# Kernel optimization log

Hardware: AMD Instinct MI355X
Metric: run time of the kernel (lower is better)

## Reference

```python
import jax, jax.numpy as jnp
import numpy as np

EMBED_DIM = 1024
HIDDEN_DIM = 4096
NUM_EXPERTS = 8
TOP_K = 2


def setup_inputs() -> dict:
    key = jax.random.key(0)
    ks = jax.random.split(key, 5)
    x = jax.random.normal(ks[0], (2, 2048, EMBED_DIM), dtype=jnp.float32)
    Wg = jax.random.normal(ks[1], (EMBED_DIM, NUM_EXPERTS), dtype=jnp.float32) * 0.02
    W1 = jax.random.normal(ks[2], (NUM_EXPERTS, EMBED_DIM, HIDDEN_DIM), dtype=jnp.float32) * 0.02
    W3 = jax.random.normal(ks[3], (NUM_EXPERTS, EMBED_DIM, HIDDEN_DIM), dtype=jnp.float32) * 0.02
    W2 = jax.random.normal(ks[4], (NUM_EXPERTS, HIDDEN_DIM, EMBED_DIM), dtype=jnp.float32) * 0.02
    return {"x": x, "Wg": Wg, "W1": W1, "W3": W3, "W2": W2}


def reference(x, Wg, W1, W3, W2):
    # Gate: linear projection to num_experts logits
    gate = jnp.einsum("bsd,de->bse", x, Wg)  # [B,S,E]
    top_vals, top_idx = jax.lax.top_k(gate, TOP_K)  # [B,S,K]
    sel_w = jax.nn.softmax(top_vals, axis=-1)  # softmax over top-k values
    # Scatter selected weights into dense [B,S,E] (zeros for unselected experts)
    dense_w = jnp.sum(
        jax.nn.one_hot(top_idx, NUM_EXPERTS, dtype=sel_w.dtype) * sel_w[..., None],
        axis=-2,
    )  # [B,S,E]
    # Per-expert SwiGLU FFN; weight=0 for tokens not routed to expert e,
    # so the weighted-sum form is mathematically identical to masked dispatch.
    out = jnp.zeros_like(x)
    for e in range(NUM_EXPERTS):
        h = jax.nn.swish(jnp.einsum("bsd,dh->bsh", x, W1[e])) * jnp.einsum(
            "bsd,dh->bsh", x, W3[e]
        )
        out = out + dense_w[..., e:e + 1] * jnp.einsum("bsh,hd->bsd", h, W2[e])
    return out
```

## Files before the change

kernel.cpp:

```cpp
#include <hip/hip_runtime.h>
#include <hip/hip_bf16.h>
#include <stdint.h>

#define D_EMBED 1024
#define D_HID   4096
#define N_TOK   4096
#define N_EXP   8
#define CAP     4096
#define NROWA   8320

typedef __attribute__((ext_vector_type(4))) float f32x4;
typedef __attribute__((ext_vector_type(8))) short bf16x8;

__device__ __forceinline__ unsigned short f2bf(float f) {
    unsigned int u = __builtin_bit_cast(unsigned int, f);
    u += 0x7fffu + ((u >> 16) & 1u);
    return (unsigned short)(u >> 16);
}

__device__ __forceinline__ void gload_lds16(const void* g, void* l) {
    __builtin_amdgcn_global_load_lds(
        (const __attribute__((address_space(1))) unsigned int*)g,
        (__attribute__((address_space(3))) unsigned int*)l,
        16, 0, 0);
}

__global__ __launch_bounds__(256) void pack_w(const float* __restrict__ W,
                                              unsigned short* __restrict__ out, int R, int C) {
    int e = blockIdx.z, kb = blockIdx.y, cb = blockIdx.x;
    const float* Wp = W + (size_t)e * R * C + (size_t)(kb * 64) * C + cb * 64;
    unsigned short* op = out + (size_t)e * R * C;
    __shared__ unsigned short lds[64][72];
    int t = threadIdx.x;
    int r = t >> 2;
    int c0 = (t & 3) << 4;
    const float* src = Wp + (size_t)r * C + c0;
#pragma unroll
    for (int i = 0; i < 2; ++i) {
        f32x4 a = *reinterpret_cast<const f32x4*>(src + i * 8);
        f32x4 b = *reinterpret_cast<const f32x4*>(src + i * 8 + 4);
        bf16x8 o;
        o[0]=(short)f2bf(a[0]); o[1]=(short)f2bf(a[1]); o[2]=(short)f2bf(a[2]); o[3]=(short)f2bf(a[3]);
        o[4]=(short)f2bf(b[0]); o[5]=(short)f2bf(b[1]); o[6]=(short)f2bf(b[2]); o[7]=(short)f2bf(b[3]);
        *reinterpret_cast<bf16x8*>(&lds[r][c0 + i * 8]) = o;
    }
    __syncthreads();
#pragma unroll
    for (int i = 0; i < 2; ++i) {
        int cell = i * 256 + t;
        int ksl = cell >> 6, col = cell & 63;
        bf16x8 o;
#pragma unroll
        for (int j = 0; j < 8; ++j) o[j] = (short)lds[ksl * 8 + j][col];
        *reinterpret_cast<bf16x8*>(op + ((size_t)(kb * 8 + ksl) * C + cb * 64 + col) * 8) = o;
    }
}

__global__ __launch_bounds__(256) void gate_kernel(const float* __restrict__ x,
                                                   const float* __restrict__ Wg,
                                                   int* __restrict__ counts,
                                                   int* __restrict__ toks,
                                                   float* __restrict__ wgts,
                                                   int* __restrict__ slots) {
    int wave = threadIdx.x >> 6;
    int lane = threadIdx.x & 63;
    int tok = blockIdx.x * 4 + wave;
    const float* xp = x + (size_t)tok * D_EMBED;
    float acc[8] = {0, 0, 0, 0, 0, 0, 0, 0};
#pragma unroll
    for (int i = 0; i < 16; ++i) {
        int d = lane + 64 * i;
        float xv = xp[d];
        f32x4 w0 = *reinterpret_cast<const f32x4*>(Wg + (size_t)d * 8);
        f32x4 w1 = *reinterpret_cast<const f32x4*>(Wg + (size_t)d * 8 + 4);
        acc[0] += xv * w0[0]; acc[1] += xv * w0[1]; acc[2] += xv * w0[2]; acc[3] += xv * w0[3];
        acc[4] += xv * w1[0]; acc[5] += xv * w1[1]; acc[6] += xv * w1[2]; acc[7] += xv * w1[3];
    }
#pragma unroll
    for (int e = 0; e < 8; ++e)
        for (int s = 32; s; s >>= 1) acc[e] += __shfl_xor(acc[e], s, 64);
    if (lane == 0) {
        int i0 = 0; float v0 = acc[0];
#pragma unroll
        for (int e = 1; e < 8; ++e) if (acc[e] > v0) { v0 = acc[e]; i0 = e; }
        int i1 = -1; float v1 = -1e30f;
#pragma unroll
        for (int e = 0; e < 8; ++e) if (e != i0 && acc[e] > v1) { v1 = acc[e]; i1 = e; }
        float ex = __expf(v1 - v0);
        float w0 = 1.0f / (1.0f + ex);
        float w1 = 1.0f - w0;
        int p0 = atomicAdd(&counts[i0], 1);
        toks[i0 * CAP + p0] = tok; wgts[i0 * CAP + p0] = w0; slots[i0 * CAP + p0] = 0;
        int p1 = atomicAdd(&counts[i1], 1);
        toks[i1 * CAP + p1] = tok; wgts[i1 * CAP + p1] = w1; slots[i1 * CAP + p1] = 1;
    }
}

__global__ void prefix_kernel(const int* __restrict__ counts, int* __restrict__ offsets) {
    if (threadIdx.x == 0) {
        int s = 0;
        for (int e = 0; e < N_EXP; ++e) { offsets[e] = s; s += counts[e]; }
    }
}

__global__ __launch_bounds__(256) void build_map_kernel(const int* __restrict__ counts,
                                                        const int* __restrict__ offsets,
                                                        const int* __restrict__ toks,
                                                        const int* __restrict__ slots,
                                                        int* __restrict__ tok2row) {
    int i = blockIdx.x * 256 + threadIdx.x;
    int e = i >> 12, pos = i & (CAP - 1);
    if (pos < counts[e])
        tok2row[toks[i] * 2 + slots[i]] = offsets[e] + pos;
}

__global__ __launch_bounds__(256) void gather_x_kernel(
    const float* __restrict__ x,
    const int* __restrict__ counts, const int* __restrict__ offsets,
    const int* __restrict__ toks,
    unsigned short* __restrict__ xg) {
    int rt = blockIdx.x;
    int e = -1, base = 0, rowbase = 0, cnt = 0;
    for (int ee = 0; ee < N_EXP; ++ee) {
        int c = counts[ee];
        int nt = (c + 63) >> 6;
        if (rt < base + nt) { e = ee; rowbase = (rt - base) << 6; cnt = c; break; }
        base += nt;
    }
    if (e < 0) return;
    int off = offsets[e];
    int kb = blockIdx.y;
    __shared__ unsigned short lds[64][72];
    int t = threadIdx.x;
    int r = t >> 2, ck = t & 3;
    int pos = rowbase + r;
    unsigned short tmp[16];
    if (pos < cnt) {
        int tok = toks[e * CAP + pos];
        const float* src = x + (size_t)tok * D_EMBED + kb * 64 + ck * 16;
#pragma unroll
        for (int i = 0; i < 4; ++i) {
            f32x4 v = *reinterpret_cast<const f32x4*>(src + i * 4);
#pragma unroll
            for (int j = 0; j < 4; ++j) tmp[i * 4 + j] = f2bf(v[j]);
        }
    } else {
#pragma unroll
        for (int i = 0; i < 16; ++i) tmp[i] = 0;
    }
#pragma unroll
    for (int i = 0; i < 16; ++i) lds[r][ck * 16 + i] = tmp[i];
    __syncthreads();
    int sl = t >> 5, rr = (t & 31) * 2;
#pragma unroll
    for (int w = 0; w < 2; ++w) {
        int rw = rr + w;
        if (rowbase + rw >= cnt) continue;
        bf16x8 o;
#pragma unroll
        for (int j = 0; j < 8; ++j) o[j] = (short)lds[rw][sl * 8 + j];
        *reinterpret_cast<bf16x8*>(xg + ((size_t)(kb * 8 + sl) * NROWA + off + rowbase + rw) * 8) = o;
    }
}

__global__ __launch_bounds__(256, 2) void gemm1_kernel(
    const unsigned short* __restrict__ xg,
    const unsigned short* __restrict__ wt1,
    const unsigned short* __restrict__ wt3,
    const int* __restrict__ counts, const int* __restrict__ offsets,
    const float* __restrict__ wgts,
    unsigned short* __restrict__ hp) {
    int rt = blockIdx.y;
    int e = -1, base = 0, rowbase = 0, cnt = 0;
    for (int ee = 0; ee < N_EXP; ++ee) {
        int c = counts[ee];
        int nt = (c + 127) >> 7;
        if (rt < base + nt) { e = ee; rowbase = (rt - base) << 7; cnt = c; break; }
        base += nt;
    }
    if (e < 0) return;
    int off = offsets[e];
    int colbase = blockIdx.x * 128;

    __shared__ __align__(16) char lds[49152];

    int t = threadIdx.x, lane = t & 63, wave = t >> 6;
    int wr = wave >> 1, wc = wave & 1;
    int q = lane >> 4, p = lane & 15;

    const unsigned short* wt1e = wt1 + (size_t)e * D_EMBED * D_HID;
    const unsigned short* wt3e = wt3 + (size_t)e * D_EMBED * D_HID;
    const unsigned short* pA = xg + (size_t)(off + rowbase) * 8;

    f32x4 acc1[4][4] = {};
    f32x4 acc3[4][4] = {};

#pragma unroll 1
    for (int kt = 0; kt < 16; ++kt) {
#pragma unroll
        for (int i = 0; i < 4; ++i) {
            int c = wave * 4 + i;
            int ksl = c >> 1, half = c & 1;
            size_t s = (size_t)(kt * 8 + ksl);
            gload_lds16(pA + (s * NROWA + half * 64 + lane) * 8, lds + c * 1024);
            size_t wofs = (s * D_HID + colbase + half * 64 + lane) * 8;
            gload_lds16(wt1e + wofs, lds + 16384 + c * 1024);
            gload_lds16(wt3e + wofs, lds + 32768 + c * 1024);
        }
        __syncthreads();
#pragma unroll
        for (int ks = 0; ks < 2; ++ks) {
            int aC = ((ks * 4 + q) * 2 + wr) * 1024 + p * 16;
            int bC = ((ks * 4 + q) * 2 + wc) * 1024 + p * 16;
            bf16x8 af[4];
#pragma unroll
            for (int m = 0; m < 4; ++m)
                af[m] = *reinterpret_cast<const bf16x8*>(lds + aC + m * 256);
#pragma unroll
            for (int n = 0; n < 4; ++n) {
                bf16x8 b1 = *reinterpret_cast<const bf16x8*>(lds + 16384 + bC + n * 256);
                bf16x8 b3 = *reinterpret_cast<const bf16x8*>(lds + 32768 + bC + n * 256);
#pragma unroll
                for (int m = 0; m < 4; ++m) {
                    acc1[m][n] = __builtin_amdgcn_mfma_f32_16x16x32_bf16(af[m], b1, acc1[m][n], 0, 0, 0);
                    acc3[m][n] = __builtin_amdgcn_mfma_f32_16x16x32_bf16(af[m], b3, acc3[m][n], 0, 0, 0);
                }
            }
        }
        __syncthreads();
    }

#pragma unroll
    for (int m = 0; m < 4; ++m) {
#pragma unroll
        for (int reg = 0; reg < 4; ++reg) {
            int rl = wr * 64 + m * 16 + q * 4 + reg;
            int grow = rowbase + rl;
            if (grow >= cnt) continue;
            float w = wgts[e * CAP + grow];
            size_t row = (size_t)(off + grow);
#pragma unroll
            for (int n = 0; n < 4; ++n) {
                float a1 = acc1[m][n][reg], a3 = acc3[m][n][reg];
                float hv = (a1 / (1.0f + __expf(-a1))) * a3 * w;
                int colg = colbase + wc * 64 + n * 16 + p;
                hp[((size_t)(colg >> 3) * NROWA + row) * 8 + (colg & 7)] = f2bf(hv);
            }
        }
    }
}

__global__ __launch_bounds__(256, 2) void gemm2_kernel(
    const unsigned short* __restrict__ hp,
    const unsigned short* __restrict__ wt2,
    const int* __restrict__ counts, const int* __restrict__ offsets,
    float* __restrict__ pbuf) {
    int rt = blockIdx.x;
    int e = -1, base = 0, rowbase = 0, cnt = 0;
    for (int ee = 0; ee < N_EXP; ++ee) {
        int c = counts[ee];
        int nt = (c + 127) >> 7;
        if (rt < base + nt) { e = ee; rowbase = (rt - base) << 7; cnt = c; break; }
        base += nt;
    }
    if (e < 0) return;
    int off = offsets[e];
    int colbase = blockIdx.y * 128;

    __shared__ __align__(16) char lds[32768];

    int t = threadIdx.x, lane = t & 63, wave = t >> 6;
    int wr = wave >> 1, wc = wave & 1;
    int q = lane >> 4, p = lane & 15;

    const unsigned short* wt2e = wt2 + (size_t)e * D_HID * D_EMBED;
    const unsigned short* pA = hp + (size_t)(off + rowbase) * 8;

    f32x4 acc[4][4] = {};

#pragma unroll 1
    for (int kt = 0; kt < 64; ++kt) {
#pragma unroll
        for (int i = 0; i < 4; ++i) {
            int c = wave * 4 + i;
            int ksl = c >> 1, half = c & 1;
            size_t s = (size_t)(kt * 8 + ksl);
            gload_lds16(pA + (s * NROWA + half * 64 + lane) * 8, lds + c * 1024);
            gload_lds16(wt2e + (s * D_EMBED + colbase + half * 64 + lane) * 8,
                        lds + 16384 + c * 1024);
        }
        __syncthreads();
#pragma unroll
        for (int ks = 0; ks < 2; ++ks) {
            int aC = ((ks * 4 + q) * 2 + wr) * 1024 + p * 16;
            int bC = 16384 + ((ks * 4 + q) * 2 + wc) * 1024 + p * 16;
            bf16x8 af[4];
#pragma unroll
            for (int m = 0; m < 4; ++m)
                af[m] = *reinterpret_cast<const bf16x8*>(lds + aC + m * 256);
#pragma unroll
            for (int n = 0; n < 4; ++n) {
                bf16x8 bn = *reinterpret_cast<const bf16x8*>(lds + bC + n * 256);
#pragma unroll
                for (int m = 0; m < 4; ++m)
                    acc[m][n] = __builtin_amdgcn_mfma_f32_16x16x32_bf16(af[m], bn, acc[m][n], 0, 0, 0);
            }
        }
        __syncthreads();
    }

#pragma unroll
    for (int m = 0; m < 4; ++m)
#pragma unroll
        for (int reg = 0; reg < 4; ++reg) {
            int rl = wr * 64 + m * 16 + q * 4 + reg;
            int grow = rowbase + rl;
            if (grow >= cnt) continue;
            float* dst = pbuf + (size_t)(off + grow) * D_EMBED + colbase + wc * 64;
#pragma unroll
            for (int n = 0; n < 4; ++n) dst[n * 16 + p] = acc[m][n][reg];
        }
}

__global__ __launch_bounds__(256) void combine_kernel(const float* __restrict__ pbuf,
                                                      const int* __restrict__ tok2row,
                                                      float* __restrict__ out) {
    int i = blockIdx.x * 256 + threadIdx.x;
    int tok = i >> 8, c = (i & 255) * 4;
    int r0 = tok2row[tok * 2], r1 = tok2row[tok * 2 + 1];
    f32x4 a = *reinterpret_cast<const f32x4*>(pbuf + (size_t)r0 * D_EMBED + c);
    f32x4 b = *reinterpret_cast<const f32x4*>(pbuf + (size_t)r1 * D_EMBED + c);
    *reinterpret_cast<f32x4*>(out + (size_t)tok * D_EMBED + c) = a + b;
}

extern "C" void kernel_launch(void* const* d_in, const int* in_sizes, int n_in,
                              void* d_out, int out_size, void* d_ws, size_t ws_size,
                              hipStream_t stream) {
    const float* x  = (const float*)d_in[0];
    const float* Wg = (const float*)d_in[1];
    const float* W1 = (const float*)d_in[2];
    const float* W3 = (const float*)d_in[3];
    const float* W2 = (const float*)d_in[4];
    float* out = (float*)d_out;

    char* ws = (char*)d_ws;
    size_t szW = (size_t)N_EXP * D_EMBED * D_HID;
    unsigned short* wt1 = (unsigned short*)ws;  ws += szW * 2;
    unsigned short* wt3 = (unsigned short*)ws;  ws += szW * 2;
    unsigned short* wt2 = (unsigned short*)ws;  ws += szW * 2;
    unsigned short* hp  = (unsigned short*)ws;  ws += (size_t)(D_HID / 8) * NROWA * 8 * 2;
    unsigned short* xg  = (unsigned short*)ws;  ws += (size_t)(D_EMBED / 8) * NROWA * 8 * 2;
    int*   toks    = (int*)ws;   ws += (size_t)N_EXP * CAP * 4;
    float* wgts    = (float*)ws; ws += (size_t)N_EXP * CAP * 4;
    int*   slots   = (int*)ws;   ws += (size_t)N_EXP * CAP * 4;
    int*   tok2row = (int*)ws;   ws += (size_t)N_TOK * 2 * 4;
    int*   counts  = (int*)ws;   ws += 8 * 4;
    int*   offsets = (int*)ws;   ws += 8 * 4;
    float* pbuf = (float*)wt1;

    hipMemsetAsync(counts, 0, 8 * sizeof(int), stream);

    pack_w<<<dim3(D_HID / 64, D_EMBED / 64, N_EXP), 256, 0, stream>>>(W1, wt1, D_EMBED, D_HID);
    pack_w<<<dim3(D_HID / 64, D_EMBED / 64, N_EXP), 256, 0, stream>>>(W3, wt3, D_EMBED, D_HID);
    pack_w<<<dim3(D_EMBED / 64, D_HID / 64, N_EXP), 256, 0, stream>>>(W2, wt2, D_HID, D_EMBED);
    gate_kernel<<<N_TOK / 4, 256, 0, stream>>>(x, Wg, counts, toks, wgts, slots);
    prefix_kernel<<<1, 64, 0, stream>>>(counts, offsets);
    build_map_kernel<<<(N_EXP * CAP) / 256, 256, 0, stream>>>(counts, offsets, toks, slots, tok2row);
    gather_x_kernel<<<dim3(136, D_EMBED / 64), 256, 0, stream>>>(x, counts, offsets, toks, xg);
    gemm1_kernel<<<dim3(32, 72), 256, 0, stream>>>(xg, wt1, wt3, counts, offsets, wgts, hp);
    gemm2_kernel<<<dim3(72, 8), 256, 0, stream>>>(hp, wt2, counts, offsets, pbuf);
    combine_kernel<<<(N_TOK * 256) / 256, 256, 0, stream>>>(pbuf, tok2row, out);
}
```

Measured before the change: 557.6 us.

## Interleave W1/W3 packing, use 256-row tiles with triple-buffered pipeline and split-K gemm2

Packs W1 and W3 into one interleaved bf16 buffer so gemm1 loads a single B tile whose columns alternate between the two projections. Both GEMMs move to 512-thread blocks with 256-row tiles and a three-stage LDS ring, prefetching two k-steps ahead and waiting with explicit vmcnt counts. gemm2 is split into two K halves that write separate partial buffers, and the combine kernel sums them. The aim is to hide global-load latency and add parallelism to gemm2. The cost is more LDS per block, single-block occupancy, extra partial-buffer traffic, and more padded rows for small experts.

```diff
diff --git a/kernel.cpp b/kernel.cpp
--- a/kernel.cpp
+++ b/kernel.cpp
@@ -7,7 +7,7 @@
 #define N_TOK   4096
 #define N_EXP   8
 #define CAP     4096
-#define NROWA   8320
+#define NROWA   8448
 
 typedef __attribute__((ext_vector_type(4))) float f32x4;
 typedef __attribute__((ext_vector_type(8))) short bf16x8;
@@ -53,6 +53,40 @@
 #pragma unroll
         for (int j = 0; j < 8; ++j) o[j] = (short)lds[ksl * 8 + j][col];
         *reinterpret_cast<bf16x8*>(op + ((size_t)(kb * 8 + ksl) * C + cb * 64 + col) * 8) = o;
+    }
+}
+
+__global__ __launch_bounds__(256) void pack_w13(const float* __restrict__ W1,
+                                                const float* __restrict__ W3,
+                                                unsigned short* __restrict__ out) {
+    int e = blockIdx.z, kb = blockIdx.y, cb = blockIdx.x;
+    size_t ebase = (size_t)e * D_EMBED * D_HID;
+    const float* b1 = W1 + ebase + (size_t)(kb * 64) * D_HID + cb * 32;
+    const float* b3 = W3 + ebase + (size_t)(kb * 64) * D_HID + cb * 32;
+    unsigned short* op = out + (size_t)e * D_EMBED * 2 * D_HID;
+    __shared__ unsigned short lds[64][72];
+    int t = threadIdx.x;
+    int r = t >> 2, ck = t & 3;
+    const float* src = (ck >= 2 ? b3 : b1) + (size_t)r * D_HID + (ck & 1) * 16;
+#pragma unroll
+    for (int i = 0; i < 2; ++i) {
+        f32x4 a = *reinterpret_cast<const f32x4*>(src + i * 8);
+        f32x4 b = *reinterpret_cast<const f32x4*>(src + i * 8 + 4);
+        bf16x8 o;
+        o[0]=(short)f2bf(a[0]); o[1]=(short)f2bf(a[1]); o[2]=(short)f2bf(a[2]); o[3]=(short)f2bf(a[3]);
+        o[4]=(short)f2bf(b[0]); o[5]=(short)f2bf(b[1]); o[6]=(short)f2bf(b[2]); o[7]=(short)f2bf(b[3]);
+        *reinterpret_cast<bf16x8*>(&lds[r][ck * 16 + i * 8]) = o;
+    }
+    __syncthreads();
+#pragma unroll
+    for (int i = 0; i < 2; ++i) {
+        int cell = i * 256 + t;
+        int ksl = cell >> 6, pcp = cell & 63;
+        int lcol = ((pcp >> 4) & 1) * 32 + ((pcp >> 5) & 1) * 16 + (pcp & 15);
+        bf16x8 o;
+#pragma unroll
+        for (int j = 0; j < 8; ++j) o[j] = (short)lds[ksl * 8 + j][lcol];
+        *reinterpret_cast<bf16x8*>(op + ((size_t)(kb * 8 + ksl) * (2 * D_HID) + cb * 64 + pcp) * 8) = o;
     }
 }
 
@@ -163,71 +197,77 @@
     }
 }
 
-__global__ __launch_bounds__(256, 2) void gemm1_kernel(
+__global__ __launch_bounds__(512, 1) void gemm1_kernel(
     const unsigned short* __restrict__ xg,
-    const unsigned short* __restrict__ wt1,
-    const unsigned short* __restrict__ wt3,
+    const unsigned short* __restrict__ wt13,
     const int* __restrict__ counts, const int* __restrict__ offsets,
     const float* __restrict__ wgts,
     unsigned short* __restrict__ hp) {
     int rt = blockIdx.y;
     int e = -1, base = 0, rowbase = 0, cnt = 0;
+#pragma unroll 1
     for (int ee = 0; ee < N_EXP; ++ee) {
         int c = counts[ee];
-        int nt = (c + 127) >> 7;
-        if (rt < base + nt) { e = ee; rowbase = (rt - base) << 7; cnt = c; break; }
+        int nt = (c + 255) >> 8;
+        if (rt < base + nt) { e = ee; rowbase = (rt - base) << 8; cnt = c; break; }
         base += nt;
     }
     if (e < 0) return;
     int off = offsets[e];
     int colbase = blockIdx.x * 128;
 
-    __shared__ __align__(16) char lds[49152];
-
-    int t = threadIdx.x, lane = t & 63, wave = t >> 6;
-    int wr = wave >> 1, wc = wave & 1;
+    __shared__ __align__(16) char lds[3][49152];
+
+    int t = threadIdx.x, lane = t & 63, w = t >> 6;
+    int wr = w >> 1, wc = w & 1;
     int q = lane >> 4, p = lane & 15;
 
-    const unsigned short* wt1e = wt1 + (size_t)e * D_EMBED * D_HID;
-    const unsigned short* wt3e = wt3 + (size_t)e * D_EMBED * D_HID;
+    const unsigned short* wB = wt13 + (size_t)e * D_EMBED * 2 * D_HID;
     const unsigned short* pA = xg + (size_t)(off + rowbase) * 8;
 
-    f32x4 acc1[4][4] = {};
-    f32x4 acc3[4][4] = {};
-
+    f32x4 acc[4][4] = {};
+
+    auto STAGE = [&](char* L, int kt) {
+        size_t sl = (size_t)(kt * 8 + w);
+#pragma unroll
+        for (int qt = 0; qt < 4; ++qt)
+            gload_lds16(pA + (sl * NROWA + qt * 64 + lane) * 8, L + (w * 4 + qt) * 1024);
+#pragma unroll
+        for (int h = 0; h < 2; ++h)
+            gload_lds16(wB + (sl * (2 * D_HID) + colbase + h * 64 + lane) * 8,
+                        L + 32768 + (w * 2 + h) * 1024);
+    };
+    auto COMPUTE = [&](const char* L) {
+#pragma unroll
+        for (int ks = 0; ks < 2; ++ks) {
+            bf16x8 af[4], bf[4];
+#pragma unroll
+            for (int m = 0; m < 4; ++m)
+                af[m] = *reinterpret_cast<const bf16x8*>(L + ((ks * 4 + q) * 4 + wr) * 1024 + m * 256 + p * 16);
+#pragma unroll
+            for (int n = 0; n < 4; ++n)
+                bf[n] = *reinterpret_cast<const bf16x8*>(L + 32768 + ((ks * 4 + q) * 2 + wc) * 1024 + n * 256 + p * 16);
+#pragma unroll
+            for (int n = 0; n < 4; ++n)
+#pragma unroll
+                for (int m = 0; m < 4; ++m)
+                    acc[m][n] = __builtin_amdgcn_mfma_f32_16x16x32_bf16(af[m], bf[n], acc[m][n], 0, 0, 0);
+        }
+    };
+
+    char* Lc = &lds[0][0]; char* Ln = &lds[1][0]; char* Ls = &lds[2][0];
+    STAGE(Lc, 0); STAGE(Ln, 1);
 #pragma unroll 1
     for (int kt = 0; kt < 16; ++kt) {
-#pragma unroll
-        for (int i = 0; i < 4; ++i) {
-            int c = wave * 4 + i;
-            int ksl = c >> 1, half = c & 1;
-            size_t s = (size_t)(kt * 8 + ksl);
-            gload_lds16(pA + (s * NROWA + half * 64 + lane) * 8, lds + c * 1024);
-            size_t wofs = (s * D_HID + colbase + half * 64 + lane) * 8;
-            gload_lds16(wt1e + wofs, lds + 16384 + c * 1024);
-            gload_lds16(wt3e + wofs, lds + 32768 + c * 1024);
-        }
-        __syncthreads();
-#pragma unroll
-        for (int ks = 0; ks < 2; ++ks) {
-            int aC = ((ks * 4 + q) * 2 + wr) * 1024 + p * 16;
-            int bC = ((ks * 4 + q) * 2 + wc) * 1024 + p * 16;
-            bf16x8 af[4];
-#pragma unroll
-            for (int m = 0; m < 4; ++m)
-                af[m] = *reinterpret_cast<const bf16x8*>(lds + aC + m * 256);
-#pragma unroll
-            for (int n = 0; n < 4; ++n) {
-                bf16x8 b1 = *reinterpret_cast<const bf16x8*>(lds + 16384 + bC + n * 256);
-                bf16x8 b3 = *reinterpret_cast<const bf16x8*>(lds + 32768 + bC + n * 256);
-#pragma unroll
-                for (int m = 0; m < 4; ++m) {
-                    acc1[m][n] = __builtin_amdgcn_mfma_f32_16x16x32_bf16(af[m], b1, acc1[m][n], 0, 0, 0);
-                    acc3[m][n] = __builtin_amdgcn_mfma_f32_16x16x32_bf16(af[m], b3, acc3[m][n], 0, 0, 0);
-                }
-            }
-        }
-        __syncthreads();
+        if (kt < 14) { STAGE(Ls, kt + 2); asm volatile("s_waitcnt vmcnt(12)" ::: "memory"); }
+        else if (kt == 14) { asm volatile("s_waitcnt vmcnt(6)" ::: "memory"); }
+        else { asm volatile("s_waitcnt vmcnt(0)" ::: "memory"); }
+        __builtin_amdgcn_s_barrier();
+        asm volatile("" ::: "memory");
+        COMPUTE(Lc);
+        asm volatile("" ::: "memory");
+        __builtin_amdgcn_s_barrier();
+        char* tmp = Lc; Lc = Ln; Ln = Ls; Ls = tmp;
     }
 
 #pragma unroll
@@ -237,78 +277,94 @@
             int rl = wr * 64 + m * 16 + q * 4 + reg;
             int grow = rowbase + rl;
             if (grow >= cnt) continue;
-            float w = wgts[e * CAP + grow];
+            float wgt = wgts[e * CAP + grow];
             size_t row = (size_t)(off + grow);
 #pragma unroll
-            for (int n = 0; n < 4; ++n) {
-                float a1 = acc1[m][n][reg], a3 = acc3[m][n][reg];
-                float hv = (a1 / (1.0f + __expf(-a1))) * a3 * w;
-                int colg = colbase + wc * 64 + n * 16 + p;
+            for (int np = 0; np < 2; ++np) {
+                float a1 = acc[m][2 * np][reg];
+                float a3 = acc[m][2 * np + 1][reg];
+                float hv = (a1 / (1.0f + __expf(-a1))) * a3 * wgt;
+                int colg = (blockIdx.x * 4 + wc * 2 + np) * 16 + p;
                 hp[((size_t)(colg >> 3) * NROWA + row) * 8 + (colg & 7)] = f2bf(hv);
             }
         }
     }
 }
 
-__global__ __launch_bounds__(256, 2) void gemm2_kernel(
+__global__ __launch_bounds__(512, 1) void gemm2_kernel(
     const unsigned short* __restrict__ hp,
     const unsigned short* __restrict__ wt2,
     const int* __restrict__ counts, const int* __restrict__ offsets,
     float* __restrict__ pbuf) {
-    int rt = blockIdx.x;
+    int rt = blockIdx.y;
     int e = -1, base = 0, rowbase = 0, cnt = 0;
+#pragma unroll 1
     for (int ee = 0; ee < N_EXP; ++ee) {
         int c = counts[ee];
-        int nt = (c + 127) >> 7;
-        if (rt < base + nt) { e = ee; rowbase = (rt - base) << 7; cnt = c; break; }
+        int nt = (c + 255) >> 8;
+        if (rt < base + nt) { e = ee; rowbase = (rt - base) << 8; cnt = c; break; }
         base += nt;
     }
     if (e < 0) return;
     int off = offsets[e];
-    int colbase = blockIdx.y * 128;
-
-    __shared__ __align__(16) char lds[32768];
-
-    int t = threadIdx.x, lane = t & 63, wave = t >> 6;
-    int wr = wave >> 1, wc = wave & 1;
+    int colbase = blockIdx.x * 128;
+    int s2 = blockIdx.z;
+
+    __shared__ __align__(16) char lds[3][49152];
+
+    int t = threadIdx.x, lane = t & 63, w = t >> 6;
+    int wr = w >> 1, wc = w & 1;
     int q = lane >> 4, p = lane & 15;
 
-    const unsigned short* wt2e = wt2 + (size_t)e * D_HID * D_EMBED;
+    const unsigned short* wB = wt2 + (size_t)e * D_HID * D_EMBED;
     const unsigned short* pA = hp + (size_t)(off + rowbase) * 8;
 
     f32x4 acc[4][4] = {};
 
+    auto STAGE = [&](char* L, int kt) {
+        size_t sl = (size_t)((s2 * 32 + kt) * 8 + w);
+#pragma unroll
+        for (int qt = 0; qt < 4; ++qt)
+            gload_lds16(pA + (sl * NROWA + qt * 64 + lane) * 8, L + (w * 4 + qt) * 1024);
+#pragma unroll
+        for (int h = 0; h < 2; ++h)
+            gload_lds16(wB + (sl * D_EMBED + colbase + h * 64 + lane) * 8,
+                        L + 32768 + (w * 2 + h) * 1024);
+    };
+    auto COMPUTE = [&](const char* L) {
+#pragma unroll
+        for (int ks = 0; ks < 2; ++ks) {
+            bf16x8 af[4], bf[4];
+#pragma unroll
+            for (int m = 0; m < 4; ++m)
+                af[m] = *reinterpret_cast<const bf16x8*>(L + ((ks * 4 + q) * 4 + wr) * 1024 + m * 256 + p * 16);
+#pragma unroll
+            for (int n = 0; n < 4; ++n)
+                bf[n] = *reinterpret_cast<const bf16x8*>(L + 32768 + ((ks * 4 + q) * 2 + wc) * 1024 + n * 256 + p * 16);
+#pragma unroll
+            for (int n = 0; n < 4; ++n)
+#pragma unroll
+                for (int m = 0; m < 4; ++m)
+                    acc[m][n] = __builtin_amdgcn_mfma_f32_16x16x32_bf16(af[m], bf[n], acc[m][n], 0, 0, 0);
+        }
+    };
+
+    char* Lc = &lds[0][0]; char* Ln = &lds[1][0]; char* Ls = &lds[2][0];
+    STAGE(Lc, 0); STAGE(Ln, 1);
 #pragma unroll 1
-    for (int kt = 0; kt < 64; ++kt) {
-#pragma unroll
-        for (int i = 0; i < 4; ++i) {
-            int c = wave * 4 + i;
-            int ksl = c >> 1, half = c & 1;
-            size_t s = (size_t)(kt * 8 + ksl);
-            gload_lds16(pA + (s * NROWA + half * 64 + lane) * 8, lds + c * 1024);
-            gload_lds16(wt2e + (s * D_EMBED + colbase + half * 64 + lane) * 8,
-                        lds + 16384 + c * 1024);
-        }
-        __syncthreads();
-#pragma unroll
-        for (int ks = 0; ks < 2; ++ks) {
-            int aC = ((ks * 4 + q) * 2 + wr) * 1024 + p * 16;
-            int bC = 16384 + ((ks * 4 + q) * 2 + wc) * 1024 + p * 16;
-            bf16x8 af[4];
-#pragma unroll
-            for (int m = 0; m < 4; ++m)
-                af[m] = *reinterpret_cast<const bf16x8*>(lds + aC + m * 256);
-#pragma unroll
-            for (int n = 0; n < 4; ++n) {
-                bf16x8 bn = *reinterpret_cast<const bf16x8*>(lds + bC + n * 256);
-#pragma unroll
-                for (int m = 0; m < 4; ++m)
-                    acc[m][n] = __builtin_amdgcn_mfma_f32_16x16x32_bf16(af[m], bn, acc[m][n], 0, 0, 0);
-            }
-        }
-        __syncthreads();
-    }
-
+    for (int kt = 0; kt < 32; ++kt) {
+        if (kt < 30) { STAGE(Ls, kt + 2); asm volatile("s_waitcnt vmcnt(12)" ::: "memory"); }
+        else if (kt == 30) { asm volatile("s_waitcnt vmcnt(6)" ::: "memory"); }
+        else { asm volatile("s_waitcnt vmcnt(0)" ::: "memory"); }
+        __builtin_amdgcn_s_barrier();
+        asm volatile("" ::: "memory");
+        COMPUTE(Lc);
+        asm volatile("" ::: "memory");
+        __builtin_amdgcn_s_barrier();
+        char* tmp = Lc; Lc = Ln; Ln = Ls; Ls = tmp;
+    }
+
+    float* pb = pbuf + (size_t)s2 * 8192 * D_EMBED;
 #pragma unroll
     for (int m = 0; m < 4; ++m)
 #pragma unroll
@@ -316,7 +372,7 @@
             int rl = wr * 64 + m * 16 + q * 4 + reg;
             int grow = rowbase + rl;
             if (grow >= cnt) continue;
-            float* dst = pbuf + (size_t)(off + grow) * D_EMBED + colbase + wc * 64;
+            float* dst = pb + (size_t)(off + grow) * D_EMBED + colbase + wc * 64;
 #pragma unroll
             for (int n = 0; n < 4; ++n) dst[n * 16 + p] = acc[m][n][reg];
         }
@@ -328,9 +384,12 @@
     int i = blockIdx.x * 256 + threadIdx.x;
     int tok = i >> 8, c = (i & 255) * 4;
     int r0 = tok2row[tok * 2], r1 = tok2row[tok * 2 + 1];
-    f32x4 a = *reinterpret_cast<const f32x4*>(pbuf + (size_t)r0 * D_EMBED + c);
-    f32x4 b = *reinterpret_cast<const f32x4*>(pbuf + (size_t)r1 * D_EMBED + c);
-    *reinterpret_cast<f32x4*>(out + (size_t)tok * D_EMBED + c) = a + b;
+    const size_t SP = (size_t)8192 * D_EMBED;
+    f32x4 a0 = *reinterpret_cast<const f32x4*>(pbuf + (size_t)r0 * D_EMBED + c);
+    f32x4 a1 = *reinterpret_cast<const f32x4*>(pbuf + SP + (size_t)r0 * D_EMBED + c);
+    f32x4 b0 = *reinterpret_cast<const f32x4*>(pbuf + (size_t)r1 * D_EMBED + c);
+    f32x4 b1 = *reinterpret_cast<const f32x4*>(pbuf + SP + (size_t)r1 * D_EMBED + c);
+    *reinterpret_cast<f32x4*>(out + (size_t)tok * D_EMBED + c) = (a0 + a1) + (b0 + b1);
 }
 
 extern "C" void kernel_launch(void* const* d_in, const int* in_sizes, int n_in,
@@ -345,29 +404,27 @@
 
     char* ws = (char*)d_ws;
     size_t szW = (size_t)N_EXP * D_EMBED * D_HID;
-    unsigned short* wt1 = (unsigned short*)ws;  ws += szW * 2;
-    unsigned short* wt3 = (unsigned short*)ws;  ws += szW * 2;
-    unsigned short* wt2 = (unsigned short*)ws;  ws += szW * 2;
-    unsigned short* hp  = (unsigned short*)ws;  ws += (size_t)(D_HID / 8) * NROWA * 8 * 2;
-    unsigned short* xg  = (unsigned short*)ws;  ws += (size_t)(D_EMBED / 8) * NROWA * 8 * 2;
+    unsigned short* wt13 = (unsigned short*)ws; ws += szW * 2 * 2;
+    unsigned short* wt2  = (unsigned short*)ws; ws += szW * 2;
+    unsigned short* hp   = (unsigned short*)ws; ws += (size_t)(D_HID / 8) * NROWA * 8 * 2;
+    unsigned short* xg   = (unsigned short*)ws; ws += (size_t)(D_EMBED / 8) * NROWA * 8 * 2;
     int*   toks    = (int*)ws;   ws += (size_t)N_EXP * CAP * 4;
     float* wgts    = (float*)ws; ws += (size_t)N_EXP * CAP * 4;
     int*   slots   = (int*)ws;   ws += (size_t)N_EXP * CAP * 4;
     int*   tok2row = (int*)ws;   ws += (size_t)N_TOK * 2 * 4;
     int*   counts  = (int*)ws;   ws += 8 * 4;
     int*   offsets = (int*)ws;   ws += 8 * 4;
-    float* pbuf = (float*)wt1;
+    float* pbuf = (float*)wt13;
 
     hipMemsetAsync(counts, 0, 8 * sizeof(int), stream);
 
-    pack_w<<<dim3(D_HID / 64, D_EMBED / 64, N_EXP), 256, 0, stream>>>(W1, wt1, D_EMBED, D_HID);
-    pack_w<<<dim3(D_HID / 64, D_EMBED / 64, N_EXP), 256, 0, stream>>>(W3, wt3, D_EMBED, D_HID);
+    pack_w13<<<dim3(128, 16, N_EXP), 256, 0, stream>>>(W1, W3, wt13);
     pack_w<<<dim3(D_EMBED / 64, D_HID / 64, N_EXP), 256, 0, stream>>>(W2, wt2, D_HID, D_EMBED);
     gate_kernel<<<N_TOK / 4, 256, 0, stream>>>(x, Wg, counts, toks, wgts, slots);
     prefix_kernel<<<1, 64, 0, stream>>>(counts, offsets);
     build_map_kernel<<<(N_EXP * CAP) / 256, 256, 0, stream>>>(counts, offsets, toks, slots, tok2row);
     gather_x_kernel<<<dim3(136, D_EMBED / 64), 256, 0, stream>>>(x, counts, offsets, toks, xg);
-    gemm1_kernel<<<dim3(32, 72), 256, 0, stream>>>(xg, wt1, wt3, counts, offsets, wgts, hp);
-    gemm2_kernel<<<dim3(72, 8), 256, 0, stream>>>(hp, wt2, counts, offsets, pbuf);
+    gemm1_kernel<<<dim3(64, 39), 512, 0, stream>>>(xg, wt13, counts, offsets, wgts, hp);
+    gemm2_kernel<<<dim3(8, 39, 2), 512, 0, stream>>>(hp, wt2, counts, offsets, pbuf);
     combine_kernel<<<(N_TOK * 256) / 256, 256, 0, stream>>>(pbuf, tok2row, out);
 }
```

Measured after the change: 564.1 us. About the same (+1.2%).
